# Optimization experiments

Hardware: AMD Instinct MI355X
Metric: run time of the kernel (lower is better)

The kernel has to match this reference:

```python
import jax, jax.numpy as jnp
import numpy as np

N_NODES = 100000
N_EDGES = 1000000
D = 128          # in_features
C = 86           # out_classes (DDI relation types)


def setup_inputs() -> dict:
    key = jax.random.key(0)
    k_h, k_src, k_dst, k_w1, k_b1, k_w2, k_b2 = jax.random.split(key, 7)
    h = jax.random.normal(k_h, (N_NODES, D), dtype=jnp.float32)
    src = jax.random.randint(k_src, (N_EDGES,), 0, N_NODES, dtype=jnp.int64)
    dst = jax.random.randint(k_dst, (N_EDGES,), 0, N_NODES, dtype=jnp.int64)
    # nn.Linear default init: U(-1/sqrt(fan_in), 1/sqrt(fan_in))
    lim1 = 1.0 / np.sqrt(2 * D)
    W1 = jax.random.uniform(k_w1, (2 * D, D), jnp.float32, -lim1, lim1)
    b1 = jax.random.uniform(k_b1, (D,), jnp.float32, -lim1, lim1)
    lim2 = 1.0 / np.sqrt(D)
    W2 = jax.random.uniform(k_w2, (D, C), jnp.float32, -lim2, lim2)
    b2 = jax.random.uniform(k_b2, (C,), jnp.float32, -lim2, lim2)
    return {"h": h, "W1": W1, "b1": b1, "W2": W2, "b2": b2,
            "src": src, "dst": dst}


def reference(h, W1, b1, W2, b2, src, dst):
    # Gather per-edge src/dst node features: [E, D] each
    h_u = h[src]
    h_v = h[dst]
    # Split W1 along its input dim instead of materializing concat [E, 2D]
    # (same math as cat([h_u, h_v], 1) @ W1)
    W1u, W1v = W1[:D], W1[D:]
    hid = jax.nn.relu(h_u @ W1u + h_v @ W1v + b1)   # [E, D]
    score = hid @ W2 + b2                            # [E, C]
    return score
```

## Files before the change

kernel.cpp:

```cpp
#include <hip/hip_runtime.h>


typedef short bf16x8 __attribute__((ext_vector_type(8)));
typedef float f32x4 __attribute__((ext_vector_type(4)));

#define DIM 128
#define C_OUT 86
#define NPAD 96
#define HSTRIDE 136

__device__ __forceinline__ float bf2f(unsigned short u) {
    unsigned int x = ((unsigned int)u) << 16;
    float f;
    __builtin_memcpy(&f, &x, 4);
    return f;
}
__device__ __forceinline__ unsigned short f2bf(float f) {
    unsigned int x;
    __builtin_memcpy(&x, &f, 4);
    x = x + 0x7fffu + ((x >> 16) & 1u);
    return (unsigned short)(x >> 16);
}

__global__ __launch_bounds__(256) void node_gemm_kernel(
    const float* __restrict__ h, const float* __restrict__ W1,
    unsigned short* __restrict__ PQ, int n_nodes)
{
    __shared__ float As[64][33];
    __shared__ float Bs[32][64];
    const int t = threadIdx.x;
    const int m0 = blockIdx.x * 64;
    const int n0 = blockIdx.y * 64;
    const float* Bbase = (n0 < 128) ? (W1 + n0) : (W1 + 128 * 128 + (n0 - 128));
    const int tx = t & 15, ty = t >> 4;
    float acc[4][4] = {};
    for (int k0 = 0; k0 < 128; k0 += 32) {
#pragma unroll
        for (int i = 0; i < 2; ++i) {
            int f = t + i * 256;
            int r = f >> 3;
            int kc = (f & 7) << 2;
            int gr = m0 + r;
            float4 v = make_float4(0.f, 0.f, 0.f, 0.f);
            if (gr < n_nodes) v = *(const float4*)(h + (size_t)gr * DIM + k0 + kc);
            As[r][kc + 0] = v.x; As[r][kc + 1] = v.y;
            As[r][kc + 2] = v.z; As[r][kc + 3] = v.w;
        }
#pragma unroll
        for (int i = 0; i < 2; ++i) {
            int f = t + i * 256;
            int kk = f >> 4;
            int jc = (f & 15) << 2;
            *(float4*)&Bs[kk][jc] = *(const float4*)(Bbase + (size_t)(k0 + kk) * DIM + jc);
        }
        __syncthreads();
#pragma unroll
        for (int kk = 0; kk < 32; ++kk) {
            float a[4], b[4];
#pragma unroll
            for (int r = 0; r < 4; ++r) a[r] = As[ty * 4 + r][kk];
#pragma unroll
            for (int c = 0; c < 4; ++c) b[c] = Bs[kk][tx * 4 + c];
#pragma unroll
            for (int r = 0; r < 4; ++r)
#pragma unroll
                for (int c = 0; c < 4; ++c) acc[r][c] += a[r] * b[c];
        }
        __syncthreads();
    }
#pragma unroll
    for (int r = 0; r < 4; ++r) {
        int gm = m0 + ty * 4 + r;
        if (gm < n_nodes) {
            ushort4 o = make_ushort4(f2bf(acc[r][0]), f2bf(acc[r][1]),
                                     f2bf(acc[r][2]), f2bf(acc[r][3]));
            *(ushort4*)(PQ + (size_t)gm * 256 + n0 + tx * 4) = o;
        }
    }
}

__global__ __launch_bounds__(256) void edge_mlp_kernel(
    const unsigned short* __restrict__ PQ,
    const float* __restrict__ b1,
    const float* __restrict__ W2,
    const float* __restrict__ b2,
    const int* __restrict__ src,
    const int* __restrict__ dst,
    float* __restrict__ out,
    int n_edges)
{
    __shared__ unsigned short W2T[NPAD * HSTRIDE];
    __shared__ unsigned short hidL[64 * HSTRIDE];
    __shared__ float b1s[DIM];
    __shared__ float b2s[NPAD];

    const int t = threadIdx.x;
    for (int i = t; i < NPAD * DIM; i += 256) {
        int n = i >> 7;
        int k = i & 127;
        float v = (n < C_OUT) ? W2[(size_t)k * C_OUT + n] : 0.f;
        W2T[n * HSTRIDE + k] = f2bf(v);
    }
    if (t < DIM) b1s[t] = b1[t];
    if (t < NPAD) b2s[t] = (t < C_OUT) ? b2[t] : 0.f;
    __syncthreads();

    const int lane = t & 63;
    const int wv = t >> 6;
    const int m = lane & 15;
    const int quad = lane >> 4;

    bf16x8 Bfrag[6][4];
#pragma unroll
    for (int nt = 0; nt < 6; ++nt)
#pragma unroll
        for (int kt = 0; kt < 4; ++kt)
            Bfrag[nt][kt] = *(const bf16x8*)&W2T[(nt * 16 + m) * HSTRIDE + kt * 32 + quad * 8];

    const ushort4* PQ4 = (const ushort4*)PQ;

    for (int e0 = blockIdx.x * 64; e0 < n_edges; e0 += gridDim.x * 64) {
#pragma unroll
        for (int i = 0; i < 8; ++i) {
            int qi = t + i * 256;
            int e = qi >> 5;
            int q = qi & 31;
            int edge = e0 + e;
            ushort4 hv = make_ushort4(0, 0, 0, 0);
            if (edge < n_edges) {
                int s = src[edge];
                int d = dst[edge];
                ushort4 pv = PQ4[(size_t)s * 64 + q];
                ushort4 qv = PQ4[(size_t)d * 64 + 32 + q];
                int k = q << 2;
                float4 bb = *(const float4*)&b1s[k];
                float x0 = fmaxf(bf2f(pv.x) + bf2f(qv.x) + bb.x, 0.f);
                float x1 = fmaxf(bf2f(pv.y) + bf2f(qv.y) + bb.y, 0.f);
                float x2 = fmaxf(bf2f(pv.z) + bf2f(qv.z) + bb.z, 0.f);
                float x3 = fmaxf(bf2f(pv.w) + bf2f(qv.w) + bb.w, 0.f);
                hv = make_ushort4(f2bf(x0), f2bf(x1), f2bf(x2), f2bf(x3));
            }
            *(ushort4*)&hidL[e * HSTRIDE + (q << 2)] = hv;
        }
        __syncthreads();

        bf16x8 af[4];
#pragma unroll
        for (int kt = 0; kt < 4; ++kt)
            af[kt] = *(const bf16x8*)&hidL[(wv * 16 + m) * HSTRIDE + kt * 32 + quad * 8];

#pragma unroll
        for (int nt = 0; nt < 6; ++nt) {
            f32x4 acc = {0.f, 0.f, 0.f, 0.f};
#pragma unroll
            for (int kt = 0; kt < 4; ++kt)
                acc = __builtin_amdgcn_mfma_f32_16x16x32_bf16(af[kt], Bfrag[nt][kt], acc, 0, 0, 0);
            int col = nt * 16 + m;
            if (col < C_OUT) {
                float bias = b2s[col];
                int ebase = e0 + wv * 16 + quad * 4;
#pragma unroll
                for (int r = 0; r < 4; ++r) {
                    int edge = ebase + r;
                    if (edge < n_edges)
                        out[(size_t)edge * C_OUT + col] = acc[r] + bias;
                }
            }
        }
        __syncthreads();
    }
}

extern "C" void kernel_launch(void* const* d_in, const int* in_sizes, int n_in,
                              void* d_out, int out_size, void* d_ws, size_t ws_size,
                              hipStream_t stream) {
    const float* h  = (const float*)d_in[0];
    const float* W1 = (const float*)d_in[1];
    const float* b1 = (const float*)d_in[2];
    const float* W2 = (const float*)d_in[3];
    const float* b2 = (const float*)d_in[4];
    const int* src  = (const int*)d_in[5];
    const int* dst  = (const int*)d_in[6];
    float* out = (float*)d_out;
    const int n_nodes = in_sizes[0] / DIM;
    const int n_edges = in_sizes[5];
    unsigned short* PQ = (unsigned short*)d_ws;

    node_gemm_kernel<<<dim3((n_nodes + 63) / 64, 4), 256, 0, stream>>>(h, W1, PQ, n_nodes);
    edge_mlp_kernel<<<dim3(768), 256, 0, stream>>>(PQ, b1, W2, b2, src, dst, out, n_edges);
}
```

Measured before the change: 622.5 us.

## Use MFMA for node GEMM and gather edge features directly into registers

The node projection GEMM moves from scalar FP32 FMAs to bf16 MFMA with a swizzled LDS tile, and b1 is folded into the Q half of the projection. The edge kernel now has each wave gather its own 16 edges straight into MFMA A-fragments, which removes the LDS staging buffer and both block-wide barriers. Output uses nontemporal stores and the grid size is doubled. Risks are extra bf16 rounding of h and W1, and uncoalesced 2-byte stores of PQ in the node kernel.

New measurement: 706.3 us. 13.5% more time.

```diff
diff --git a/kernel.cpp b/kernel.cpp
--- a/kernel.cpp
+++ b/kernel.cpp
@@ -24,64 +24,86 @@
 
 __global__ __launch_bounds__(256) void node_gemm_kernel(
     const float* __restrict__ h, const float* __restrict__ W1,
-    unsigned short* __restrict__ PQ, int n_nodes)
+    const float* __restrict__ b1, unsigned short* __restrict__ PQ, int n_nodes)
 {
-    __shared__ float As[64][33];
-    __shared__ float Bs[32][64];
+    __shared__ unsigned short Abf[64 * 128];
+
     const int t = threadIdx.x;
     const int m0 = blockIdx.x * 64;
-    const int n0 = blockIdx.y * 64;
-    const float* Bbase = (n0 < 128) ? (W1 + n0) : (W1 + 128 * 128 + (n0 - 128));
-    const int tx = t & 15, ty = t >> 4;
-    float acc[4][4] = {};
-    for (int k0 = 0; k0 < 128; k0 += 32) {
-#pragma unroll
-        for (int i = 0; i < 2; ++i) {
-            int f = t + i * 256;
-            int r = f >> 3;
-            int kc = (f & 7) << 2;
-            int gr = m0 + r;
-            float4 v = make_float4(0.f, 0.f, 0.f, 0.f);
-            if (gr < n_nodes) v = *(const float4*)(h + (size_t)gr * DIM + k0 + kc);
-            As[r][kc + 0] = v.x; As[r][kc + 1] = v.y;
-            As[r][kc + 2] = v.z; As[r][kc + 3] = v.w;
-        }
-#pragma unroll
-        for (int i = 0; i < 2; ++i) {
-            int f = t + i * 256;
-            int kk = f >> 4;
-            int jc = (f & 15) << 2;
-            *(float4*)&Bs[kk][jc] = *(const float4*)(Bbase + (size_t)(k0 + kk) * DIM + jc);
-        }
-        __syncthreads();
-#pragma unroll
-        for (int kk = 0; kk < 32; ++kk) {
-            float a[4], b[4];
-#pragma unroll
-            for (int r = 0; r < 4; ++r) a[r] = As[ty * 4 + r][kk];
-#pragma unroll
-            for (int c = 0; c < 4; ++c) b[c] = Bs[kk][tx * 4 + c];
-#pragma unroll
-            for (int r = 0; r < 4; ++r)
-#pragma unroll
-                for (int c = 0; c < 4; ++c) acc[r][c] += a[r] * b[c];
-        }
-        __syncthreads();
-    }
-#pragma unroll
-    for (int r = 0; r < 4; ++r) {
-        int gm = m0 + ty * 4 + r;
-        if (gm < n_nodes) {
-            ushort4 o = make_ushort4(f2bf(acc[r][0]), f2bf(acc[r][1]),
-                                     f2bf(acc[r][2]), f2bf(acc[r][3]));
-            *(ushort4*)(PQ + (size_t)gm * 256 + n0 + tx * 4) = o;
+    const int lane = t & 63;
+    const int wv = t >> 6;
+    const int m = lane & 15;
+    const int quad = lane >> 4;
+
+    bf16x8 Bf[4][4];
+    float b1v[4];
+#pragma unroll
+    for (int nt = 0; nt < 4; ++nt) {
+        int n = wv * 64 + nt * 16 + m;
+        const float* colp = (n < DIM) ? (W1 + n) : (W1 + DIM * DIM + (n - DIM));
+        b1v[nt] = (n >= DIM) ? b1[n - DIM] : 0.f;
+#pragma unroll
+        for (int kt = 0; kt < 4; ++kt) {
+            bf16x8 f;
+#pragma unroll
+            for (int j = 0; j < 8; ++j)
+                f[j] = (short)f2bf(colp[(kt * 32 + quad * 8 + j) * DIM]);
+            Bf[nt][kt] = f;
+        }
+    }
+
+#pragma unroll
+    for (int it = 0; it < 4; ++it) {
+        int i = t + it * 256;
+        int r = i >> 4;
+        int c = i & 15;
+        int gr = m0 + r;
+        float4 v0 = make_float4(0.f, 0.f, 0.f, 0.f), v1 = v0;
+        if (gr < n_nodes) {
+            const float* hp = h + (size_t)gr * DIM + c * 8;
+            v0 = *(const float4*)hp;
+            v1 = *(const float4*)(hp + 4);
+        }
+        bf16x8 o;
+        o[0] = (short)f2bf(v0.x); o[1] = (short)f2bf(v0.y);
+        o[2] = (short)f2bf(v0.z); o[3] = (short)f2bf(v0.w);
+        o[4] = (short)f2bf(v1.x); o[5] = (short)f2bf(v1.y);
+        o[6] = (short)f2bf(v1.z); o[7] = (short)f2bf(v1.w);
+        int byteoff = r * 256 + ((c * 16) ^ ((r & 7) << 4));
+        *(bf16x8*)((char*)Abf + byteoff) = o;
+    }
+    __syncthreads();
+
+#pragma unroll
+    for (int mt = 0; mt < 4; ++mt) {
+        bf16x8 af[4];
+        int row = mt * 16 + m;
+        int rs = row * 256;
+        int sw = (row & 7) << 4;
+#pragma unroll
+        for (int kt = 0; kt < 4; ++kt) {
+            int byteoff = rs + (((kt * 4 + quad) * 16) ^ sw);
+            af[kt] = *(const bf16x8*)((const char*)Abf + byteoff);
+        }
+#pragma unroll
+        for (int nt = 0; nt < 4; ++nt) {
+            f32x4 acc = {0.f, 0.f, 0.f, 0.f};
+#pragma unroll
+            for (int kt = 0; kt < 4; ++kt)
+                acc = __builtin_amdgcn_mfma_f32_16x16x32_bf16(af[kt], Bf[nt][kt], acc, 0, 0, 0);
+            int nn = wv * 64 + nt * 16 + m;
+#pragma unroll
+            for (int r = 0; r < 4; ++r) {
+                int gm = m0 + mt * 16 + quad * 4 + r;
+                if (gm < n_nodes)
+                    PQ[(size_t)gm * 256 + nn] = f2bf(acc[r] + b1v[nt]);
+            }
         }
     }
 }
 
 __global__ __launch_bounds__(256) void edge_mlp_kernel(
     const unsigned short* __restrict__ PQ,
-    const float* __restrict__ b1,
     const float* __restrict__ W2,
     const float* __restrict__ b2,
     const int* __restrict__ src,
@@ -90,8 +112,6 @@
     int n_edges)
 {
     __shared__ unsigned short W2T[NPAD * HSTRIDE];
-    __shared__ unsigned short hidL[64 * HSTRIDE];
-    __shared__ float b1s[DIM];
     __shared__ float b2s[NPAD];
 
     const int t = threadIdx.x;
@@ -101,7 +121,6 @@
         float v = (n < C_OUT) ? W2[(size_t)k * C_OUT + n] : 0.f;
         W2T[n * HSTRIDE + k] = f2bf(v);
     }
-    if (t < DIM) b1s[t] = b1[t];
     if (t < NPAD) b2s[t] = (t < C_OUT) ? b2[t] : 0.f;
     __syncthreads();
 
@@ -117,38 +136,31 @@
         for (int kt = 0; kt < 4; ++kt)
             Bfrag[nt][kt] = *(const bf16x8*)&W2T[(nt * 16 + m) * HSTRIDE + kt * 32 + quad * 8];
 
-    const ushort4* PQ4 = (const ushort4*)PQ;
-
-    for (int e0 = blockIdx.x * 64; e0 < n_edges; e0 += gridDim.x * 64) {
-#pragma unroll
-        for (int i = 0; i < 8; ++i) {
-            int qi = t + i * 256;
-            int e = qi >> 5;
-            int q = qi & 31;
-            int edge = e0 + e;
-            ushort4 hv = make_ushort4(0, 0, 0, 0);
-            if (edge < n_edges) {
-                int s = src[edge];
-                int d = dst[edge];
-                ushort4 pv = PQ4[(size_t)s * 64 + q];
-                ushort4 qv = PQ4[(size_t)d * 64 + 32 + q];
-                int k = q << 2;
-                float4 bb = *(const float4*)&b1s[k];
-                float x0 = fmaxf(bf2f(pv.x) + bf2f(qv.x) + bb.x, 0.f);
-                float x1 = fmaxf(bf2f(pv.y) + bf2f(qv.y) + bb.y, 0.f);
-                float x2 = fmaxf(bf2f(pv.z) + bf2f(qv.z) + bb.z, 0.f);
-                float x3 = fmaxf(bf2f(pv.w) + bf2f(qv.w) + bb.w, 0.f);
-                hv = make_ushort4(f2bf(x0), f2bf(x1), f2bf(x2), f2bf(x3));
+    const int gw = blockIdx.x * 4 + wv;
+    const int gstride = gridDim.x * 4 * 16;
+
+    for (int eb = gw * 16; eb < n_edges; eb += gstride) {
+        int edge = eb + m;
+        bool ev = edge < n_edges;
+        int s = ev ? src[edge] : 0;
+        int d = ev ? dst[edge] : 0;
+        const bf16x8* Pr = (const bf16x8*)(PQ + (size_t)s * 256);
+        const bf16x8* Qr = (const bf16x8*)(PQ + (size_t)d * 256 + 128);
+        bf16x8 pf[4], qf[4];
+#pragma unroll
+        for (int kt = 0; kt < 4; ++kt) {
+            pf[kt] = Pr[kt * 4 + quad];
+            qf[kt] = Qr[kt * 4 + quad];
+        }
+        bf16x8 af[4];
+#pragma unroll
+        for (int kt = 0; kt < 4; ++kt) {
+#pragma unroll
+            for (int j = 0; j < 8; ++j) {
+                float x = bf2f((unsigned short)pf[kt][j]) + bf2f((unsigned short)qf[kt][j]);
+                af[kt][j] = (short)f2bf(fmaxf(x, 0.f));
             }
-            *(ushort4*)&hidL[e * HSTRIDE + (q << 2)] = hv;
-        }
-        __syncthreads();
-
-        bf16x8 af[4];
-#pragma unroll
-        for (int kt = 0; kt < 4; ++kt)
-            af[kt] = *(const bf16x8*)&hidL[(wv * 16 + m) * HSTRIDE + kt * 32 + quad * 8];
-
+        }
 #pragma unroll
         for (int nt = 0; nt < 6; ++nt) {
             f32x4 acc = {0.f, 0.f, 0.f, 0.f};
@@ -158,16 +170,16 @@
             int col = nt * 16 + m;
             if (col < C_OUT) {
                 float bias = b2s[col];
-                int ebase = e0 + wv * 16 + quad * 4;
+                int ebase = eb + quad * 4;
 #pragma unroll
                 for (int r = 0; r < 4; ++r) {
-                    int edge = ebase + r;
-                    if (edge < n_edges)
-                        out[(size_t)edge * C_OUT + col] = acc[r] + bias;
+                    int e2 = ebase + r;
+                    if (e2 < n_edges)
+                        __builtin_nontemporal_store(acc[r] + bias,
+                                                    &out[(size_t)e2 * C_OUT + col]);
                 }
             }
         }
-        __syncthreads();
     }
 }
 
@@ -186,6 +198,6 @@
     const int n_edges = in_sizes[5];
     unsigned short* PQ = (unsigned short*)d_ws;
 
-    node_gemm_kernel<<<dim3((n_nodes + 63) / 64, 4), 256, 0, stream>>>(h, W1, PQ, n_nodes);
-    edge_mlp_kernel<<<dim3(768), 256, 0, stream>>>(PQ, b1, W2, b2, src, dst, out, n_edges);
-}
+    node_gemm_kernel<<<dim3((n_nodes + 63) / 64), 256, 0, stream>>>(h, W1, b1, PQ, n_nodes);
+    edge_mlp_kernel<<<dim3(1536), 256, 0, stream>>>(PQ, W2, b2, src, dst, out, n_edges);
+}
```
